# Kernel tuning notes

Measured on AMD Instinct MI355X. Metric: run time of the kernel, lower is better.

Reference implementation:

```python
import jax, jax.numpy as jnp
import numpy as np

V = 1.0e10           # large init value for non-seed pixels (FastGeodis v)
LAMB = 0.0           # lamb=0 => pure Euclidean raster-scan distance
ITERS = 2            # FastGeodis iterations
THRESH = 0.7         # binarize_map threshold
TOPO_WEIGHT = 0.005
TOPO_WINDOW = 64
EPS = 1e-6
BIG = 1e20


def _sweep_down(dist, image):
    # One top-down raster sweep of the FastGeodis up-down pass.
    # dist, image: [H, W]. Row r updates from row r-1 at col offsets {-1,0,+1}
    # with squared spatial distances {2,1,2}; lamb weights the intensity term.
    W = dist.shape[1]
    sp2 = (2.0, 1.0, 2.0)

    def step(carry, xs):
        pd, pi = carry          # previous-row distance / intensity, [W]
        d_row, i_row = xs
        pd_pad = jnp.pad(pd, 1, constant_values=BIG)
        pi_pad = jnp.pad(pi, 1, constant_values=0.0)
        new = d_row
        for k in range(3):
            p = pd_pad[k:k + W]
            q = i_row - pi_pad[k:k + W]
            new = jnp.minimum(new, p + jnp.sqrt(sp2[k] + LAMB * q * q))
        return (new, i_row), new

    (_, _), rest = jax.lax.scan(step, (dist[0], image[0]), (dist[1:], image[1:]))
    return jnp.concatenate([dist[:1], rest], axis=0)


def _updown(dist, image):
    dist = _sweep_down(dist, image)
    dist = _sweep_down(dist[::-1], image[::-1])[::-1]
    return dist


def generalised_geodesic2d(image, softmask):
    # image: intensity map [H,W]; softmask: [H,W]; dist init = V * softmask.
    dist = V * softmask
    for _ in range(ITERS):
        dist = _updown(dist, image)
        dist = _updown(dist.T, image.T).T
    return dist


def calculate_edt(inp):
    # Original: softmask = inp, intensity image = 1 - inp (mask_pt = 1 - image_pt).
    return generalised_geodesic2d(1.0 - inp, inp)


def _global_norm(x):
    return (x - x.min()) / (x.max() - x.min() + EPS)


def _topo_loss(p, t, window):
    # Persistence-style matching proxy: within each non-overlapping window,
    # match level-set values of pred and target by sorting (0-dim persistence
    # birth/death values of the filtration are order statistics of the window)
    # and penalize squared differences of matched values.
    H, W = p.shape
    nh, nw = H // window, W // window

    def win_sort(x):
        x = x.reshape(nh, window, nw, window).transpose(0, 2, 1, 3)
        return jnp.sort(x.reshape(nh * nw, window * window), axis=-1)

    return jnp.mean((win_sort(p) - win_sort(t)) ** 2)


def _per_item(pred_i, target_i):
    # pred_i/target_i: [C, H, W]; pred already remapped to [0, 1]
    bin_pred = (pred_i >= THRESH).astype(jnp.float32)
    comb_pred = jnp.max(bin_pred, axis=0)        # combine_channels
    comb_tgt = jnp.max(target_i, axis=0)
    edt_p = _global_norm(calculate_edt(1.0 - comb_pred))
    edt_t = _global_norm(calculate_edt(1.0 - comb_tgt))
    return _topo_loss(edt_p, edt_t, TOPO_WINDOW)


def setup_inputs():
    key = jax.random.key(0)
    k1, k2 = jax.random.split(key)
    B, C, H, W = 16, 3, 512, 512
    pred = jax.random.normal(k1, (B, C, H, W), dtype=jnp.float32)  # model output in ~[-1,1]
    # target: binary multi-channel cell masks (sparse foreground)
    target = (jax.random.uniform(k2, (B, C, H, W)) > 0.8).astype(jnp.float32)
    return {"pred": pred, "target": target}


def reference(pred, target):
    pred01 = (pred + 1.0) / 2.0
    losses = jax.vmap(_per_item)(pred01.astype(jnp.float32), target.astype(jnp.float32))
    mean_loss = losses.mean()
    return (mean_loss * TOPO_WEIGHT, mean_loss)
```

## Files before the change

kernel.cpp:

```cpp
#include <hip/hip_runtime.h>

#define BIGF 1e20f
#define VF   1e10f

constexpr float SQ2 = 1.41421356237309515f;

__device__ __forceinline__ float dpp_left(float x)
{
    int o = __builtin_amdgcn_update_dpp(0x60AD78ECu , __float_as_int(x),
                                        0x138, 0xF, 0xF, false);
    return __int_as_float(o);
}
__device__ __forceinline__ float dpp_right(float x)
{
    int o = __builtin_amdgcn_update_dpp(0x60AD78ECu , __float_as_int(x),
                                        0x130, 0xF, 0xF, false);
    return __int_as_float(o);
}
template<int CTRL>
__device__ __forceinline__ float qdpp(float x)
{
    return __int_as_float(__builtin_amdgcn_update_dpp(0, __float_as_int(x),
                                                      CTRL, 0xF, 0xF, true));
}
__device__ __forceinline__ float fmed3(float a, float b, float c)
{
    return __builtin_amdgcn_fmed3f(a, b, c);
}

__device__ __forceinline__ void load_row8(const float* __restrict__ M, int r, int c0, float v[8])
{
    const float4* q = (const float4*)(M + ((long)r << 9) + c0);
    float4 a = q[0], b = q[1];
    v[0] = a.x; v[1] = a.y; v[2] = a.z; v[3] = a.w;
    v[4] = b.x; v[5] = b.y; v[6] = b.z; v[7] = b.w;
}
__device__ __forceinline__ void store_row8(float* __restrict__ M, int r, int c0, const float v[8])
{
    float4* q = (float4*)(M + ((long)r << 9) + c0);
    q[0] = make_float4(v[0], v[1], v[2], v[3]);
    q[1] = make_float4(v[4], v[5], v[6], v[7]);
}

__device__ __forceinline__ void step8(const float cur[8], const float p[8], float nv[8])
{
    float left  = dpp_left(p[7]);
    float right = dpp_right(p[0]);
    #pragma unroll
    for (int j = 0; j < 8; ++j) {
        float l  = (j == 0) ? left  : p[j - 1];
        float rr = (j == 7) ? right : p[j + 1];
        nv[j] = fminf(fminf(cur[j], p[j] + 1.0f), fminf(l, rr) + SQ2);
    }
}

__global__ __launch_bounds__(256) void k_init(const float* __restrict__ pred,
                                              const float* __restrict__ tgt,
                                              float* __restrict__ bufA,
                                              float* __restrict__ acc,
                                              unsigned* __restrict__ count,
                                              float* __restrict__ minmax)
{
    if (blockIdx.x == 0 && threadIdx.x == 0) { *acc = 0.0f; *count = 0u; }
    if (blockIdx.x == 0 && threadIdx.x < 64)
        minmax[threadIdx.x] = (threadIdx.x & 1) ? 0.0f : BIGF;

    int r = blockIdx.x & 7;
    int k = blockIdx.x >> 3;
    int b = r + 8 * (k >> 8);
    int pix = ((k & 255) * 256 + threadIdx.x) << 2;
    long base = (long)b * 3 * 262144 + pix;

    float4 p0 = *(const float4*)(pred + base);
    float4 p1 = *(const float4*)(pred + base + 262144);
    float4 p2 = *(const float4*)(pred + base + 2 * 262144);
    float4 t0 = *(const float4*)(tgt + base);
    float4 t1 = *(const float4*)(tgt + base + 262144);
    float4 t2 = *(const float4*)(tgt + base + 2 * 262144);

    float P0[4] = {p0.x, p0.y, p0.z, p0.w};
    float P1[4] = {p1.x, p1.y, p1.z, p1.w};
    float P2[4] = {p2.x, p2.y, p2.z, p2.w};
    float T0[4] = {t0.x, t0.y, t0.z, t0.w};
    float T1[4] = {t1.x, t1.y, t1.z, t1.w};
    float T2[4] = {t2.x, t2.y, t2.z, t2.w};

    float oP[4], oT[4];
    #pragma unroll
    for (int e = 0; e < 4; ++e) {
        bool fgP = ((P0[e] + 1.0f) * 0.5f >= 0.7f) ||
                   ((P1[e] + 1.0f) * 0.5f >= 0.7f) ||
                   ((P2[e] + 1.0f) * 0.5f >= 0.7f);
        float mt = fmaxf(fmaxf(T0[e], T1[e]), T2[e]);
        oP[e] = fgP ? 0.0f : VF;
        oT[e] = VF * (1.0f - mt);
    }
    *(float4*)(bufA + (long)b * 262144 + pix)        = make_float4(oP[0], oP[1], oP[2], oP[3]);
    *(float4*)(bufA + (long)(16 + b) * 262144 + pix) = make_float4(oT[0], oT[1], oT[2], oT[3]);
}

__global__ __launch_bounds__(64) void k_p1d(const float* __restrict__ X0,
                                            float* __restrict__ Cb)
{
    int bi = blockIdx.x, m = bi >> 4, w = bi & 15;
    const float* X = X0 + ((long)m << 18);
    int c0 = (int)threadIdx.x << 3, a = w << 5;
    float p[8]; load_row8(X, a, c0, p);
    float buf[8][8];
    #pragma unroll
    for (int k = 1; k <= 7; ++k) load_row8(X, a + k, c0, buf[k & 7]);
    #pragma unroll
    for (int i = 1; i < 32; ++i) {
        if (i + 7 < 32) load_row8(X, a + i + 7, c0, buf[(i + 7) & 7]);
        float nv[8]; step8(buf[i & 7], p, nv);
        #pragma unroll
        for (int j = 0; j < 8; ++j) p[j] = nv[j];
    }
    float4* o = (float4*)(Cb + m * 8192 + w * 512 + c0);
    o[0] = make_float4(p[0], p[1], p[2], p[3]);
    o[1] = make_float4(p[4], p[5], p[6], p[7]);
}

__device__ __forceinline__ void combine(float* __restrict__ bwp, float* __restrict__ part,
                                        int wdst, int wsrc, int t, int wave, int lane,
                                        const float wreg[8])
{
    const float* bs = bwp + wsrc * 576;
    if (wave <= 8) {
        int base = lane * 8 + 8 * wave;
        float W[16];
        float4 W0 = *(const float4*)(bs + base);
        float4 W1 = *(const float4*)(bs + base + 4);
        W[0]=W0.x; W[1]=W0.y; W[2]=W0.z; W[3]=W0.w;
        W[4]=W1.x; W[5]=W1.y; W[6]=W1.z; W[7]=W1.w;
        float acc[8];
        if (wave < 8) {
            float4 W2 = *(const float4*)(bs + base + 8);
            float4 W3 = *(const float4*)(bs + base + 12);
            W[8]=W2.x; W[9]=W2.y; W[10]=W2.z; W[11]=W2.w;
            W[12]=W3.x; W[13]=W3.y; W[14]=W3.z; W[15]=W3.w;
            #pragma unroll
            for (int j = 0; j < 8; ++j) acc[j] = W[j] + wreg[0];
            #pragma unroll
            for (int dt = 1; dt < 8; ++dt)
                #pragma unroll
                for (int j = 0; j < 8; ++j)
                    acc[j] = fminf(acc[j], W[j + dt] + wreg[dt]);
        } else {
            #pragma unroll
            for (int j = 0; j < 8; ++j) acc[j] = W[j] + wreg[0];
        }
        float4* pp = (float4*)(part + wave * 512 + lane * 8);
        pp[0] = make_float4(acc[0], acc[1], acc[2], acc[3]);
        pp[1] = make_float4(acc[4], acc[5], acc[6], acc[7]);
    }
    __syncthreads();
    if (t < 512) {
        float r = bwp[wdst * 576 + 32 + t];
        #pragma unroll
        for (int p2 = 0; p2 < 9; ++p2) r = fminf(r, part[p2 * 512 + t]);
        bwp[wdst * 576 + 32 + t] = r;
    }
    __syncthreads();
}

__global__ __launch_bounds__(1024) void k_comb(float* __restrict__ Cb, int dir)
{
    __shared__ __align__(16) float bwp[16 * 576];
    __shared__ __align__(16) float part[9 * 512];
    __shared__ float wgt[72];
    int m = blockIdx.x, t = threadIdx.x, wave = t >> 6, lane = t & 63, c0 = lane << 3;
    float* Cm = Cb + m * 8192;

    bwp[wave * 576 + ((lane < 32) ? lane : lane + 512)] = BIGF;
    *(float4*)(bwp + wave * 576 + 32 + c0)     = *(const float4*)(Cm + wave * 512 + c0);
    *(float4*)(bwp + wave * 576 + 32 + c0 + 4) = *(const float4*)(Cm + wave * 512 + c0 + 4);
    if (t < 65) { int d = t - 32; int ad = d < 0 ? -d : d; wgt[t] = ad * SQ2 + (float)(32 - ad); }
    __syncthreads();
    float wreg[8];
    #pragma unroll
    for (int dt = 0; dt < 8; ++dt) wreg[dt] = BIGF;
    if (wave < 8) {
        #pragma unroll
        for (int dt = 0; dt < 8; ++dt) wreg[dt] = wgt[wave * 8 + dt];
    } else if (wave == 8) wreg[0] = wgt[64];

    #pragma unroll 1
    for (int i = 0; i < 15; ++i) {
        int w2 = (dir > 0) ? (1 + i) : (14 - i);
        combine(bwp, part, w2, w2 - dir, t, wave, lane, wreg);
    }
    *(float4*)(Cm + wave * 512 + c0)     = *(const float4*)(bwp + wave * 576 + 32 + c0);
    *(float4*)(Cm + wave * 512 + c0 + 4) = *(const float4*)(bwp + wave * 576 + 32 + c0 + 4);
}

__global__ __launch_bounds__(64) void k_p3d1u(const float* __restrict__ X0,
                                              float* __restrict__ Y0,
                                              const float* __restrict__ Cb,
                                              float* __restrict__ Db)
{
    __shared__ __align__(16) float stash[31 * 512];
    int bi = blockIdx.x, m = bi >> 4, w = bi & 15;
    const float* X = X0 + ((long)m << 18);
    float* Y = Y0 + ((long)m << 18);
    const int L = threadIdx.x;
    int c0 = L << 3, a = w << 5;
    float p[8], buf[8][8];

    if (w == 0) {
        load_row8(X, 0, c0, p);
        store_row8(Y, 0, c0, p);
        *(float4*)(stash + 0 * 512 + L * 4)       = make_float4(p[0], p[1], p[2], p[3]);
        *(float4*)(stash + 0 * 512 + 256 + L * 4) = make_float4(p[4], p[5], p[6], p[7]);
        #pragma unroll
        for (int k = 1; k <= 7; ++k) load_row8(X, k, c0, buf[k & 7]);
        #pragma unroll
        for (int i = 1; i < 32; ++i) {
            if (i + 7 < 32) load_row8(X, i + 7, c0, buf[(i + 7) & 7]);
            float nv[8]; step8(buf[i & 7], p, nv);
            store_row8(Y, i, c0, nv);
            if (i < 31) {
                *(float4*)(stash + i * 512 + L * 4)       = make_float4(nv[0], nv[1], nv[2], nv[3]);
                *(float4*)(stash + i * 512 + 256 + L * 4) = make_float4(nv[4], nv[5], nv[6], nv[7]);
            }
            #pragma unroll
            for (int j = 0; j < 8; ++j) p[j] = nv[j];
        }
    } else {
        const float4* s = (const float4*)(Cb + m * 8192 + (w - 1) * 512 + c0);
        float4 s0 = s[0], s1 = s[1];
        p[0]=s0.x; p[1]=s0.y; p[2]=s0.z; p[3]=s0.w;
        p[4]=s1.x; p[5]=s1.y; p[6]=s1.z; p[7]=s1.w;
        #pragma unroll
        for (int k = 0; k < 7; ++k) load_row8(X, a + k, c0, buf[k & 7]);
        #pragma unroll
        for (int i = 0; i < 32; ++i) {
            if (i + 7 < 32) load_row8(X, a + i + 7, c0, buf[(i + 7) & 7]);
            float nv[8]; step8(buf[i & 7], p, nv);
            store_row8(Y, a + i, c0, nv);
            if (i < 31) {
                *(float4*)(stash + i * 512 + L * 4)       = make_float4(nv[0], nv[1], nv[2], nv[3]);
                *(float4*)(stash + i * 512 + 256 + L * 4) = make_float4(nv[4], nv[5], nv[6], nv[7]);
            }
            #pragma unroll
            for (int j = 0; j < 8; ++j) p[j] = nv[j];
        }
    }

    float q[8], cur[8];
    #pragma unroll
    for (int j = 0; j < 8; ++j) q[j] = p[j];
    {
        float4 x0 = *(const float4*)(stash + 30 * 512 + L * 4);
        float4 x1 = *(const float4*)(stash + 30 * 512 + 256 + L * 4);
        cur[0]=x0.x; cur[1]=x0.y; cur[2]=x0.z; cur[3]=x0.w;
        cur[4]=x1.x; cur[5]=x1.y; cur[6]=x1.z; cur[7]=x1.w;
    }
    #pragma unroll
    for (int i = 1; i < 32; ++i) {
        float nxt[8];
        if (i < 31) {
            float4 x0 = *(const float4*)(stash + (30 - i) * 512 + L * 4);
            float4 x1 = *(const float4*)(stash + (30 - i) * 512 + 256 + L * 4);
            nxt[0]=x0.x; nxt[1]=x0.y; nxt[2]=x0.z; nxt[3]=x0.w;
            nxt[4]=x1.x; nxt[5]=x1.y; nxt[6]=x1.z; nxt[7]=x1.w;
        }
        float nv[8]; step8(cur, q, nv);
        #pragma unroll
        for (int j = 0; j < 8; ++j) q[j] = nv[j];
        if (i < 31) {
            #pragma unroll
            for (int j = 0; j < 8; ++j) cur[j] = nxt[j];
        }
    }
    float4* o = (float4*)(Db + m * 8192 + w * 512 + c0);
    o[0] = make_float4(q[0], q[1], q[2], q[3]);
    o[1] = make_float4(q[4], q[5], q[6], q[7]);
}

__device__ __forceinline__ void tile_store(float* tile, int h, int c0, const float v[8])
{
    float4* q = (float4*)(tile + h * 516 + c0);
    q[0] = make_float4(v[0], v[1], v[2], v[3]);
    q[1] = make_float4(v[4], v[5], v[6], v[7]);
}
__device__ __forceinline__ void half_out(const float* tile, float* __restrict__ Xo,
                                         int a2, int L)
{
    int g = L >> 2, j = (L & 3) << 2;
    #pragma unroll
    for (int it = 0; it < 32; ++it) {
        int c = (it << 4) + g;
        float4 v = make_float4(tile[(j + 0) * 516 + c], tile[(j + 1) * 516 + c],
                               tile[(j + 2) * 516 + c], tile[(j + 3) * 516 + c]);
        *(float4*)(Xo + (long)c * 512 + a2 + j) = v;
    }
}

__global__ __launch_bounds__(64) void k_p3u(const float* __restrict__ Y0,
                                            float* __restrict__ Xo0,
                                            const float* __restrict__ Db,
                                            float* __restrict__ minmax,
                                            int final_pass)
{
    __shared__ __align__(16) float tile[16 * 516];
    int bi = blockIdx.x, m = bi >> 4, w = bi & 15;
    const float* Y = Y0 + ((long)m << 18);
    float* Xo = Xo0 + ((long)m << 18);
    int L = threadIdx.x, c0 = L << 3, a = w << 5;
    float p[8], buf[8][8];
    float mn = BIGF, mx = -BIGF;

    if (w == 15) {
        load_row8(Y, 511, c0, p);
        tile_store(tile, 15, c0, p);
        #pragma unroll
        for (int j = 0; j < 8; ++j) { mn = fminf(mn, p[j]); mx = fmaxf(mx, p[j]); }
        #pragma unroll
        for (int k = 1; k <= 3; ++k) load_row8(Y, 511 - k, c0, buf[k & 3]);
        #pragma unroll
        for (int i = 1; i < 16; ++i) {
            load_row8(Y, 511 - (i + 3), c0, buf[(i + 3) & 3]);
            float nv[8]; step8(buf[i & 3], p, nv);
            tile_store(tile, 15 - i, c0, nv);
            #pragma unroll
            for (int j = 0; j < 8; ++j) { p[j] = nv[j]; mn = fminf(mn, nv[j]); mx = fmaxf(mx, nv[j]); }
        }
        half_out(tile, Xo, a + 16, L);
        #pragma unroll
        for (int i = 16; i < 32; ++i) {
            if (i + 3 < 32) load_row8(Y, 511 - (i + 3), c0, buf[(i + 3) & 3]);
            float nv[8]; step8(buf[i & 3], p, nv);
            tile_store(tile, 31 - i, c0, nv);
            #pragma unroll
            for (int j = 0; j < 8; ++j) { p[j] = nv[j]; mn = fminf(mn, nv[j]); mx = fmaxf(mx, nv[j]); }
        }
        half_out(tile, Xo, a, L);
    } else {
        const float4* s = (const float4*)(Db + m * 8192 + (w + 1) * 512 + c0);
        float4 s0 = s[0], s1 = s[1];
        p[0]=s0.x; p[1]=s0.y; p[2]=s0.z; p[3]=s0.w;
        p[4]=s1.x; p[5]=s1.y; p[6]=s1.z; p[7]=s1.w;
        #pragma unroll
        for (int k = 0; k < 3; ++k) load_row8(Y, a + 31 - k, c0, buf[k & 3]);
        #pragma unroll
        for (int i = 0; i < 16; ++i) {
            load_row8(Y, a + 31 - (i + 3), c0, buf[(i + 3) & 3]);
            float nv[8]; step8(buf[i & 3], p, nv);
            tile_store(tile, 15 - i, c0, nv);
            #pragma unroll
            for (int j = 0; j < 8; ++j) { p[j] = nv[j]; mn = fminf(mn, nv[j]); mx = fmaxf(mx, nv[j]); }
        }
        half_out(tile, Xo, a + 16, L);
        #pragma unroll
        for (int i = 16; i < 32; ++i) {
            if (i + 3 < 32) load_row8(Y, a + 31 - (i + 3), c0, buf[(i + 3) & 3]);
            float nv[8]; step8(buf[i & 3], p, nv);
            tile_store(tile, 31 - i, c0, nv);
            #pragma unroll
            for (int j = 0; j < 8; ++j) { p[j] = nv[j]; mn = fminf(mn, nv[j]); mx = fmaxf(mx, nv[j]); }
        }
        half_out(tile, Xo, a, L);
    }

    if (final_pass) {
        for (int o = 32; o > 0; o >>= 1) {
            mn = fminf(mn, __shfl_down(mn, o));
            mx = fmaxf(mx, __shfl_down(mx, o));
        }
        if (L == 0) {
            atomicMin((int*)(minmax + 2 * m),     __float_as_int(mn));
            atomicMax((int*)(minmax + 2 * m + 1), __float_as_int(mx));
        }
    }
}

__device__ __forceinline__ void cex(float& lo, float& hi)
{
    float l = fminf(lo, hi);
    hi = fmaxf(lo, hi);
    lo = l;
}
__device__ __forceinline__ void merge8asc(float v[8])
{
    cex(v[0],v[4]); cex(v[1],v[5]); cex(v[2],v[6]); cex(v[3],v[7]);
    cex(v[0],v[2]); cex(v[1],v[3]); cex(v[4],v[6]); cex(v[5],v[7]);
    cex(v[0],v[1]); cex(v[2],v[3]); cex(v[4],v[5]); cex(v[6],v[7]);
}
__device__ __forceinline__ void sort8asc(float v[8])
{
    cex(v[0],v[1]); cex(v[2],v[3]); cex(v[4],v[5]); cex(v[6],v[7]);
    cex(v[0],v[3]); cex(v[1],v[2]); cex(v[4],v[7]); cex(v[5],v[6]);
    cex(v[0],v[1]); cex(v[2],v[3]); cex(v[4],v[5]); cex(v[6],v[7]);
    cex(v[0],v[7]); cex(v[1],v[6]); cex(v[2],v[5]); cex(v[3],v[4]);
    cex(v[0],v[2]); cex(v[1],v[3]); cex(v[4],v[6]); cex(v[5],v[7]);
    cex(v[0],v[1]); cex(v[2],v[3]); cex(v[4],v[5]); cex(v[6],v[7]);
}
__device__ __forceinline__ void xshfl(float v[8], int j8, float sel)
{
    #pragma unroll
    for (int e = 0; e < 8; ++e) {
        float o = __shfl_xor(v[e], j8);
        v[e] = fmed3(v[e], o, sel);
    }
}
template<int CTRL>
__device__ __forceinline__ void xdpp(float v[8], float sel)
{
    #pragma unroll
    for (int e = 0; e < 8; ++e) {
        float o = qdpp<CTRL>(v[e]);
        v[e] = fmed3(v[e], o, sel);
    }
}
__device__ __forceinline__ void rshfl(float v[8], int tmask, float sel)
{
    float o[8];
    #pragma unroll
    for (int e = 0; e < 8; ++e) o[e] = __shfl_xor(v[7 - e], tmask);
    #pragma unroll
    for (int e = 0; e < 8; ++e) v[e] = fmed3(v[e], o[e], sel);
}
template<int CTRL>
__device__ __forceinline__ void rdpp(float v[8], float sel)
{
    float o[8];
    #pragma unroll
    for (int e = 0; e < 8; ++e) o[e] = qdpp<CTRL>(v[7 - e]);
    #pragma unroll
    for (int e = 0; e < 8; ++e) v[e] = fmed3(v[e], o[e], sel);
}
__device__ __forceinline__ void lstage(float p[8], float q[8], int tmask, float sel, bool rev,
                                       float* sp, float* st, int t)
{
    __syncthreads();
    int sw = (t >> 2) & 1;
    int o0 = t * 8 + sw * 4;
    int o1 = t * 8 + (sw ^ 1) * 4;
    *(float4*)(sp + o0) = make_float4(p[0], p[1], p[2], p[3]);
    *(float4*)(sp + o1) = make_float4(p[4], p[5], p[6], p[7]);
    *(float4*)(st + o0) = make_float4(q[0], q[1], q[2], q[3]);
    *(float4*)(st + o1) = make_float4(q[4], q[5], q[6], q[7]);
    __syncthreads();
    int pt = t ^ tmask;
    int psw = (pt >> 2) & 1;
    int q0 = pt * 8 + psw * 4;
    int q1 = pt * 8 + (psw ^ 1) * 4;
    float4 a = *(const float4*)(sp + q0), bb = *(const float4*)(sp + q1);
    float4 c = *(const float4*)(st + q0), d = *(const float4*)(st + q1);
    float op[8] = {a.x,a.y,a.z,a.w,bb.x,bb.y,bb.z,bb.w};
    float oq[8] = {c.x,c.y,c.z,c.w,d.x,d.y,d.z,d.w};
    if (rev) {
        #pragma unroll
        for (int e = 0; e < 8; ++e) {
            p[e] = fmed3(p[e], op[7 - e], sel);
            q[e] = fmed3(q[e], oq[7 - e], sel);
        }
    } else {
        #pragma unroll
        for (int e = 0; e < 8; ++e) {
            p[e] = fmed3(p[e], op[e], sel);
            q[e] = fmed3(q[e], oq[e], sel);
        }
    }
}

__global__ __launch_bounds__(512) void k_loss(const float* __restrict__ bufB,
                                              const float* __restrict__ minmax,
                                              float* __restrict__ acc,
                                              unsigned* __restrict__ count,
                                              float* __restrict__ out)
{
    __shared__ float sp[4096];
    __shared__ float st[4096];
    __shared__ float rs[8];

    int t = threadIdx.x;
    int r = blockIdx.x & 7;
    int k = blockIdx.x >> 3;
    int b = r + 8 * (k >> 6);
    int w = k & 63;
    int wi = w >> 3, wj = w & 7;

    int i0 = t << 3;
    int y = wi * 64 + (i0 >> 6);
    int x = wj * 64 + (i0 & 63);

    float mnP = minmax[2 * b],        mxP = minmax[2 * b + 1];
    float mnT = minmax[2 * (16 + b)], mxT = minmax[2 * (16 + b) + 1];
    float sclP = 1.0f / (mxP - mnP + 1e-6f);
    float sclT = 1.0f / (mxT - mnT + 1e-6f);

    float p[8], q[8];
    {
        const float4* P4 = (const float4*)(bufB + (long)b * 262144 + y * 512 + x);
        const float4* T4 = (const float4*)(bufB + (long)(16 + b) * 262144 + y * 512 + x);
        float4 a = P4[0], bb = P4[1], c = T4[0], d = T4[1];
        p[0]=a.x; p[1]=a.y; p[2]=a.z; p[3]=a.w; p[4]=bb.x; p[5]=bb.y; p[6]=bb.z; p[7]=bb.w;
        q[0]=c.x; q[1]=c.y; q[2]=c.z; q[3]=c.w; q[4]=d.x;  q[5]=d.y;  q[6]=d.z;  q[7]=d.w;
        #pragma unroll
        for (int e = 0; e < 8; ++e) {
            p[e] = (p[e] - mnP) * sclP;
            q[e] = (q[e] - mnT) * sclT;
        }
    }

    const float INFP = __builtin_inff();
    sort8asc(p); sort8asc(q);

    #pragma unroll 1
    for (int kk = 16; kk <= 4096; kk <<= 1) {
        int tmask = (kk - 1) >> 3;
        float sel = ((t & (kk >> 4)) == 0) ? -INFP : INFP;
        if (kk == 16)        { rdpp<0xB1>(p, sel); rdpp<0xB1>(q, sel); }
        else if (kk == 32)   { rdpp<0x1B>(p, sel); rdpp<0x1B>(q, sel); }
        else if (tmask < 64) { rshfl(p, tmask, sel); rshfl(q, tmask, sel); }
        else                 lstage(p, q, tmask, sel, true, sp, st, t);

        #pragma unroll 1
        for (int j = kk >> 2; j >= 8; j >>= 1) {
            int j8 = j >> 3;
            float s2 = ((t & j8) == 0) ? -INFP : INFP;
            if (j8 == 1)      { xdpp<0xB1>(p, s2); xdpp<0xB1>(q, s2); }
            else if (j8 == 2) { xdpp<0x4E>(p, s2); xdpp<0x4E>(q, s2); }
            else if (j8 < 64) { xshfl(p, j8, s2); xshfl(q, j8, s2); }
            else              lstage(p, q, j8, s2, false, sp, st, t);
        }
        merge8asc(p); merge8asc(q);
    }

    float s = 0.0f;
    #pragma unroll
    for (int e = 0; e < 8; ++e) { float d = p[e] - q[e]; s += d * d; }
    for (int o = 32; o > 0; o >>= 1) s += __shfl_down(s, o);
    if ((t & 63) == 0) rs[t >> 6] = s;
    __syncthreads();
    if (t == 0) {
        float tot = 0.0f;
        #pragma unroll
        for (int i = 0; i < 8; ++i) tot += rs[i];
        atomicAdd(acc, tot);
        __threadfence();
        unsigned done = atomicAdd(count, 1u);
        if (done == 1023u) {
            float total = atomicAdd(acc, 0.0f);
            float mean = total * (1.0f / 4194304.0f);
            out[0] = mean * 0.005f;
            out[1] = mean;
        }
    }
}

extern "C" void kernel_launch(void* const* d_in, const int* in_sizes, int n_in,
                              void* d_out, int out_size, void* d_ws, size_t ws_size,
                              hipStream_t stream)
{
    const float* pred = (const float*)d_in[0];
    const float* tgt  = (const float*)d_in[1];
    float* out = (float*)d_out;

    char* ws = (char*)d_ws;
    float* bufA     = (float*)ws;
    float* bufB     = (float*)(ws + (32ull << 20));
    float* Cb       = (float*)(ws + (64ull << 20));
    float* Db       = (float*)(ws + (65ull << 20));
    float* minmax   = (float*)(ws + (66ull << 20));
    float* acc      = minmax + 64;
    unsigned* count = (unsigned*)(acc + 1);

    k_init<<<4096, 256, 0, stream>>>(pred, tgt, bufA, acc, count, minmax);

    for (int s = 0; s < 4; ++s) {
        k_p1d  <<<512,   64, 0, stream>>>(bufA, Cb);
        k_comb <<< 32, 1024, 0, stream>>>(Cb, +1);
        k_p3d1u<<<512,   64, 0, stream>>>(bufA, bufB, Cb, Db);
        k_comb <<< 32, 1024, 0, stream>>>(Db, -1);
        k_p3u  <<<512,   64, 0, stream>>>(bufB, bufA, Db, minmax, s == 3 ? 1 : 0);
    }

    k_loss<<<1024, 512, 0, stream>>>(bufA, minmax, acc, count, out);
}
```

Measured before the change: 392.2 us.

## Recompute down sweep in final kernel instead of storing intermediate buffer

The middle kernel no longer writes the full down-swept image to global memory; it only computes the boundary rows for the up-sweep carries. The final kernel re-reads the original input, recomputes the down sweep from the Cb carries into shared memory, then runs the up sweep from LDS and writes the transposed output. The input and output buffers now ping-pong between iterations. This removes one full-image global write and read per stage, at the cost of recomputing the down sweep and using a larger shared-memory stash.

```diff
diff --git a/kernel.cpp b/kernel.cpp
--- a/kernel.cpp
+++ b/kernel.cpp
@@ -34,12 +34,6 @@
     float4 a = q[0], b = q[1];
     v[0] = a.x; v[1] = a.y; v[2] = a.z; v[3] = a.w;
     v[4] = b.x; v[5] = b.y; v[6] = b.z; v[7] = b.w;
-}
-__device__ __forceinline__ void store_row8(float* __restrict__ M, int r, int c0, const float v[8])
-{
-    float4* q = (float4*)(M + ((long)r << 9) + c0);
-    q[0] = make_float4(v[0], v[1], v[2], v[3]);
-    q[1] = make_float4(v[4], v[5], v[6], v[7]);
 }
 
 __device__ __forceinline__ void step8(const float cur[8], const float p[8], float nv[8])
@@ -194,57 +188,39 @@
     *(float4*)(Cm + wave * 512 + c0 + 4) = *(const float4*)(bwp + wave * 576 + 32 + c0 + 4);
 }
 
-__global__ __launch_bounds__(64) void k_p3d1u(const float* __restrict__ X0,
-                                              float* __restrict__ Y0,
-                                              const float* __restrict__ Cb,
-                                              float* __restrict__ Db)
+__global__ __launch_bounds__(64) void k_pb(const float* __restrict__ X0,
+                                           const float* __restrict__ Cb,
+                                           float* __restrict__ Db)
 {
     __shared__ __align__(16) float stash[31 * 512];
     int bi = blockIdx.x, m = bi >> 4, w = bi & 15;
     const float* X = X0 + ((long)m << 18);
-    float* Y = Y0 + ((long)m << 18);
     const int L = threadIdx.x;
     int c0 = L << 3, a = w << 5;
     float p[8], buf[8][8];
 
-    if (w == 0) {
-        load_row8(X, 0, c0, p);
-        store_row8(Y, 0, c0, p);
-        *(float4*)(stash + 0 * 512 + L * 4)       = make_float4(p[0], p[1], p[2], p[3]);
-        *(float4*)(stash + 0 * 512 + 256 + L * 4) = make_float4(p[4], p[5], p[6], p[7]);
-        #pragma unroll
-        for (int k = 1; k <= 7; ++k) load_row8(X, k, c0, buf[k & 7]);
-        #pragma unroll
-        for (int i = 1; i < 32; ++i) {
-            if (i + 7 < 32) load_row8(X, i + 7, c0, buf[(i + 7) & 7]);
-            float nv[8]; step8(buf[i & 7], p, nv);
-            store_row8(Y, i, c0, nv);
-            if (i < 31) {
-                *(float4*)(stash + i * 512 + L * 4)       = make_float4(nv[0], nv[1], nv[2], nv[3]);
-                *(float4*)(stash + i * 512 + 256 + L * 4) = make_float4(nv[4], nv[5], nv[6], nv[7]);
-            }
-            #pragma unroll
-            for (int j = 0; j < 8; ++j) p[j] = nv[j];
-        }
-    } else {
+    if (w) {
         const float4* s = (const float4*)(Cb + m * 8192 + (w - 1) * 512 + c0);
         float4 s0 = s[0], s1 = s[1];
         p[0]=s0.x; p[1]=s0.y; p[2]=s0.z; p[3]=s0.w;
         p[4]=s1.x; p[5]=s1.y; p[6]=s1.z; p[7]=s1.w;
-        #pragma unroll
-        for (int k = 0; k < 7; ++k) load_row8(X, a + k, c0, buf[k & 7]);
-        #pragma unroll
-        for (int i = 0; i < 32; ++i) {
-            if (i + 7 < 32) load_row8(X, a + i + 7, c0, buf[(i + 7) & 7]);
-            float nv[8]; step8(buf[i & 7], p, nv);
-            store_row8(Y, a + i, c0, nv);
-            if (i < 31) {
-                *(float4*)(stash + i * 512 + L * 4)       = make_float4(nv[0], nv[1], nv[2], nv[3]);
-                *(float4*)(stash + i * 512 + 256 + L * 4) = make_float4(nv[4], nv[5], nv[6], nv[7]);
-            }
-            #pragma unroll
-            for (int j = 0; j < 8; ++j) p[j] = nv[j];
-        }
+    } else {
+        #pragma unroll
+        for (int j = 0; j < 8; ++j) p[j] = BIGF;
+    }
+
+    #pragma unroll
+    for (int k = 0; k < 7; ++k) load_row8(X, a + k, c0, buf[k & 7]);
+    #pragma unroll
+    for (int i = 0; i < 32; ++i) {
+        if (i + 7 < 32) load_row8(X, a + i + 7, c0, buf[(i + 7) & 7]);
+        float nv[8]; step8(buf[i & 7], p, nv);
+        if (i < 31) {
+            *(float4*)(stash + i * 512 + L * 4)       = make_float4(nv[0], nv[1], nv[2], nv[3]);
+            *(float4*)(stash + i * 512 + 256 + L * 4) = make_float4(nv[4], nv[5], nv[6], nv[7]);
+        }
+        #pragma unroll
+        for (int j = 0; j < 8; ++j) p[j] = nv[j];
     }
 
     float q[8], cur[8];
@@ -278,90 +254,104 @@
     o[1] = make_float4(q[4], q[5], q[6], q[7]);
 }
 
-__device__ __forceinline__ void tile_store(float* tile, int h, int c0, const float v[8])
-{
-    float4* q = (float4*)(tile + h * 516 + c0);
+__device__ __forceinline__ void sst516(float* st, int slot, int c0, const float v[8])
+{
+    float4* q = (float4*)(st + slot * 516 + c0);
     q[0] = make_float4(v[0], v[1], v[2], v[3]);
     q[1] = make_float4(v[4], v[5], v[6], v[7]);
 }
-__device__ __forceinline__ void half_out(const float* tile, float* __restrict__ Xo,
-                                         int a2, int L)
+__device__ __forceinline__ void sld516(const float* st, int slot, int c0, float v[8])
+{
+    const float4* q = (const float4*)(st + slot * 516 + c0);
+    float4 a = q[0], b = q[1];
+    v[0]=a.x; v[1]=a.y; v[2]=a.z; v[3]=a.w;
+    v[4]=b.x; v[5]=b.y; v[6]=b.z; v[7]=b.w;
+}
+__device__ __forceinline__ void half_out32(const float* st, float* __restrict__ Xo,
+                                           int slotbase, int a2, int L)
 {
     int g = L >> 2, j = (L & 3) << 2;
     #pragma unroll
     for (int it = 0; it < 32; ++it) {
         int c = (it << 4) + g;
-        float4 v = make_float4(tile[(j + 0) * 516 + c], tile[(j + 1) * 516 + c],
-                               tile[(j + 2) * 516 + c], tile[(j + 3) * 516 + c]);
+        float4 v = make_float4(st[(slotbase + j + 0) * 516 + c],
+                               st[(slotbase + j + 1) * 516 + c],
+                               st[(slotbase + j + 2) * 516 + c],
+                               st[(slotbase + j + 3) * 516 + c]);
         *(float4*)(Xo + (long)c * 512 + a2 + j) = v;
     }
 }
 
-__global__ __launch_bounds__(64) void k_p3u(const float* __restrict__ Y0,
+__global__ __launch_bounds__(64) void k_p3u(const float* __restrict__ X0,
                                             float* __restrict__ Xo0,
+                                            const float* __restrict__ Cb,
                                             const float* __restrict__ Db,
                                             float* __restrict__ minmax,
                                             int final_pass)
 {
-    __shared__ __align__(16) float tile[16 * 516];
+    __shared__ __align__(16) float stash[32 * 516];
     int bi = blockIdx.x, m = bi >> 4, w = bi & 15;
-    const float* Y = Y0 + ((long)m << 18);
+    const float* X = X0 + ((long)m << 18);
     float* Xo = Xo0 + ((long)m << 18);
-    int L = threadIdx.x, c0 = L << 3, a = w << 5;
+    const int L = threadIdx.x;
+    int c0 = L << 3, a = w << 5;
     float p[8], buf[8][8];
-    float mn = BIGF, mx = -BIGF;
-
-    if (w == 15) {
-        load_row8(Y, 511, c0, p);
-        tile_store(tile, 15, c0, p);
-        #pragma unroll
-        for (int j = 0; j < 8; ++j) { mn = fminf(mn, p[j]); mx = fmaxf(mx, p[j]); }
-        #pragma unroll
-        for (int k = 1; k <= 3; ++k) load_row8(Y, 511 - k, c0, buf[k & 3]);
-        #pragma unroll
-        for (int i = 1; i < 16; ++i) {
-            load_row8(Y, 511 - (i + 3), c0, buf[(i + 3) & 3]);
-            float nv[8]; step8(buf[i & 3], p, nv);
-            tile_store(tile, 15 - i, c0, nv);
-            #pragma unroll
-            for (int j = 0; j < 8; ++j) { p[j] = nv[j]; mn = fminf(mn, nv[j]); mx = fmaxf(mx, nv[j]); }
-        }
-        half_out(tile, Xo, a + 16, L);
-        #pragma unroll
-        for (int i = 16; i < 32; ++i) {
-            if (i + 3 < 32) load_row8(Y, 511 - (i + 3), c0, buf[(i + 3) & 3]);
-            float nv[8]; step8(buf[i & 3], p, nv);
-            tile_store(tile, 31 - i, c0, nv);
-            #pragma unroll
-            for (int j = 0; j < 8; ++j) { p[j] = nv[j]; mn = fminf(mn, nv[j]); mx = fmaxf(mx, nv[j]); }
-        }
-        half_out(tile, Xo, a, L);
-    } else {
-        const float4* s = (const float4*)(Db + m * 8192 + (w + 1) * 512 + c0);
+
+    if (w) {
+        const float4* s = (const float4*)(Cb + m * 8192 + (w - 1) * 512 + c0);
         float4 s0 = s[0], s1 = s[1];
         p[0]=s0.x; p[1]=s0.y; p[2]=s0.z; p[3]=s0.w;
         p[4]=s1.x; p[5]=s1.y; p[6]=s1.z; p[7]=s1.w;
-        #pragma unroll
-        for (int k = 0; k < 3; ++k) load_row8(Y, a + 31 - k, c0, buf[k & 3]);
-        #pragma unroll
-        for (int i = 0; i < 16; ++i) {
-            load_row8(Y, a + 31 - (i + 3), c0, buf[(i + 3) & 3]);
-            float nv[8]; step8(buf[i & 3], p, nv);
-            tile_store(tile, 15 - i, c0, nv);
+    } else {
+        #pragma unroll
+        for (int j = 0; j < 8; ++j) p[j] = BIGF;
+    }
+    #pragma unroll
+    for (int k = 0; k < 7; ++k) load_row8(X, a + k, c0, buf[k & 7]);
+    #pragma unroll
+    for (int i = 0; i < 32; ++i) {
+        if (i + 7 < 32) load_row8(X, a + i + 7, c0, buf[(i + 7) & 7]);
+        float nv[8]; step8(buf[i & 7], p, nv);
+        sst516(stash, i, c0, nv);
+        #pragma unroll
+        for (int j = 0; j < 8; ++j) p[j] = nv[j];
+    }
+
+    float s2[8];
+    if (w < 15) {
+        const float4* s = (const float4*)(Db + m * 8192 + (w + 1) * 512 + c0);
+        float4 s0 = s[0], s1 = s[1];
+        s2[0]=s0.x; s2[1]=s0.y; s2[2]=s0.z; s2[3]=s0.w;
+        s2[4]=s1.x; s2[5]=s1.y; s2[6]=s1.z; s2[7]=s1.w;
+    } else {
+        #pragma unroll
+        for (int j = 0; j < 8; ++j) s2[j] = BIGF;
+    }
+    float mn = BIGF, mx = -BIGF;
+    #pragma unroll
+    for (int i = 0; i < 16; ++i) {
+        float cu[8];
+        if (i == 0) {
             #pragma unroll
-            for (int j = 0; j < 8; ++j) { p[j] = nv[j]; mn = fminf(mn, nv[j]); mx = fmaxf(mx, nv[j]); }
-        }
-        half_out(tile, Xo, a + 16, L);
-        #pragma unroll
-        for (int i = 16; i < 32; ++i) {
-            if (i + 3 < 32) load_row8(Y, a + 31 - (i + 3), c0, buf[(i + 3) & 3]);
-            float nv[8]; step8(buf[i & 3], p, nv);
-            tile_store(tile, 31 - i, c0, nv);
-            #pragma unroll
-            for (int j = 0; j < 8; ++j) { p[j] = nv[j]; mn = fminf(mn, nv[j]); mx = fmaxf(mx, nv[j]); }
-        }
-        half_out(tile, Xo, a, L);
-    }
+            for (int j = 0; j < 8; ++j) cu[j] = p[j];
+        } else {
+            sld516(stash, 31 - i, c0, cu);
+        }
+        float nv[8]; step8(cu, s2, nv);
+        sst516(stash, 31 - i, c0, nv);
+        #pragma unroll
+        for (int j = 0; j < 8; ++j) { s2[j] = nv[j]; mn = fminf(mn, nv[j]); mx = fmaxf(mx, nv[j]); }
+    }
+    half_out32(stash, Xo, 16, a + 16, L);
+    #pragma unroll
+    for (int i = 16; i < 32; ++i) {
+        float cu[8]; sld516(stash, 31 - i, c0, cu);
+        float nv[8]; step8(cu, s2, nv);
+        sst516(stash, 31 - i, c0, nv);
+        #pragma unroll
+        for (int j = 0; j < 8; ++j) { s2[j] = nv[j]; mn = fminf(mn, nv[j]); mx = fmaxf(mx, nv[j]); }
+    }
+    half_out32(stash, Xo, 0, a, L);
 
     if (final_pass) {
         for (int o = 32; o > 0; o >>= 1) {
@@ -571,11 +561,13 @@
     k_init<<<4096, 256, 0, stream>>>(pred, tgt, bufA, acc, count, minmax);
 
     for (int s = 0; s < 4; ++s) {
-        k_p1d  <<<512,   64, 0, stream>>>(bufA, Cb);
-        k_comb <<< 32, 1024, 0, stream>>>(Cb, +1);
-        k_p3d1u<<<512,   64, 0, stream>>>(bufA, bufB, Cb, Db);
-        k_comb <<< 32, 1024, 0, stream>>>(Db, -1);
-        k_p3u  <<<512,   64, 0, stream>>>(bufB, bufA, Db, minmax, s == 3 ? 1 : 0);
+        const float* in = (s & 1) ? bufB : bufA;
+        float* outb     = (s & 1) ? bufA : bufB;
+        k_p1d <<<512,   64, 0, stream>>>(in, Cb);
+        k_comb<<< 32, 1024, 0, stream>>>(Cb, +1);
+        k_pb  <<<512,   64, 0, stream>>>(in, Cb, Db);
+        k_comb<<< 32, 1024, 0, stream>>>(Db, -1);
+        k_p3u <<<512,   64, 0, stream>>>(in, outb, Cb, Db, minmax, s == 3 ? 1 : 0);
     }
 
     k_loss<<<1024, 512, 0, stream>>>(bufA, minmax, acc, count, out);
```

New measurement: 385.7 us. No clear change (-1.7%).
